# Kernel tuning notes

Hardware: AMD Instinct MI355X
Metric: run time of the kernel (lower is better)

The kernel has to match this reference:

```python
import jax, jax.numpy as jnp
import numpy as np

BS, HS, NH = 8, 3, 8          # block_size, halo_size, num_heads
WIN = BS + 2 * HS             # 14
DQK = 16                      # dim_head_qk = make_divisible(128*1.0)//8
DV = 16                       # dim_head_v = 128 // 8
SCALE = DQK ** -0.5


def _rel_pos_index():
    # Faithful numpy port of QueryFreePosEmbedRel._get_relative_position_index
    w = WIN
    coords = np.stack(np.meshgrid(np.arange(w), np.arange(w), indexing='ij'))  # (2,w,w)
    flat = coords.reshape(2, -1)                                               # (2, w*w)
    rel = flat[:, :, None] - flat[:, None, :]                                  # (2, ww, ww)
    rel = rel.transpose(1, 2, 0).astype(np.int64)
    rel[:, :, 0] += w - 1
    rel[:, :, 1] += w - 1
    rel[:, :, 0] *= 2 * w - 1
    rel = rel.sum(-1).reshape(w, w, w, w)
    sh = (w - BS) // 2  # == halo_size
    rel = rel[sh:sh + BS, sh:sh + BS, :, :].reshape(BS * BS, w * w)
    return rel

_REL_IDX = _rel_pos_index()


def setup_inputs() -> dict:
    key = jax.random.key(0)
    k1, k2, k3, k4, k5, k6 = jax.random.split(key, 6)
    C = 128
    dim_out_qk = NH * DQK   # 128
    dim_out_v = NH * DV     # 128
    x = jax.random.normal(k1, (4, 128, 128, C), dtype=jnp.float32)
    q_w = jax.random.normal(k2, (dim_out_qk, C), dtype=jnp.float32) * 0.05
    kv_w = jax.random.normal(k3, (dim_out_qk + dim_out_v, C), dtype=jnp.float32) * 0.05
    pos_table = jax.random.normal(k4, ((2 * WIN - 1) * (2 * WIN - 1), NH), dtype=jnp.float32) * 0.02
    proj_w = jax.random.normal(k5, (dim_out_v, dim_out_v), dtype=jnp.float32) * 0.05
    proj_b = jax.random.normal(k6, (dim_out_v,), dtype=jnp.float32) * 0.01
    return {"x": x, "q_w": q_w, "kv_w": kv_w, "pos_table": pos_table,
            "proj_w": proj_w, "proj_b": proj_b}


def reference(x, q_w, kv_w, pos_table, proj_w, proj_b):
    B, H, W, C = x.shape  # H,W divisible by BS -> no padding branch
    nhb, nwb = H // BS, W // BS
    nb = nhb * nwb

    # --- queries: (B,NH,nb,bs^2,DQK), block-partitioned ---
    q = x @ q_w.T
    q = q.reshape(B, nhb, BS, nwb, BS, NH, DQK).transpose(0, 5, 1, 3, 2, 4, 6)
    q = q.reshape(B, NH, nb, BS * BS, DQK)

    # --- kv 1x1 conv + halo padding + overlapping window extraction ---
    kv = x @ kv_w.T                                   # (B,H,W, NH*(DQK+DV))
    kv = jnp.pad(kv, ((0, 0), (HS, HS), (HS, HS), (0, 0)))
    ri = (np.arange(nhb) * BS)[:, None] + np.arange(WIN)[None, :]
    ci = (np.arange(nwb) * BS)[:, None] + np.arange(WIN)[None, :]
    kvw = kv[:, ri]
    kvw = kvw[:, :, :, ci]
    kvw = kvw.transpose(0, 1, 3, 2, 4, 5).reshape(B, nb, WIN * WIN, NH, DQK + DV)
    kvw = kvw.transpose(0, 3, 1, 2, 4)
    k = kvw[..., :DQK]
    v = kvw[..., DQK:]

    bias = pos_table[_REL_IDX.reshape(-1)].reshape(BS * BS, WIN * WIN, NH)
    bias = bias.transpose(2, 0, 1)[None, :, None]

    # --- scores + halo-boundary mask + softmax ---
    attn = jnp.einsum('bhnqd,bhnkd->bhnqk', q * SCALE, k) + bias
    ones = jnp.pad(jnp.ones((H, W), jnp.float32), ((HS, HS), (HS, HS)))
    mw = ones[ri][:, :, ci].transpose(0, 2, 1, 3).reshape(nb, WIN * WIN)
    valid = (mw > 0)[None, None, :, None, :]
    attn = jnp.where(valid, attn, -jnp.finfo(attn.dtype).max)
    attn = jax.nn.softmax(attn, axis=-1)

    # --- weighted sum over V, fold blocks back to (B,H,W,dim_out_v) ---
    out = jnp.einsum('bhnqk,bhnkd->bhnqd', attn, v)   # (B,NH,nb,bs^2,DV)
    out = out.reshape(B, NH, nhb, nwb, BS, BS, DV)
    out = out.transpose(0, 2, 4, 3, 5, 1, 6).reshape(B, H, W, NH * DV)
    return out @ proj_w.T + proj_b
```

## Files before the change

kernel.cpp:

```cpp
#include <hip/hip_runtime.h>
#include <float.h>


typedef float f32x4 __attribute__((ext_vector_type(4)));
typedef short s16x4 __attribute__((ext_vector_type(4)));
typedef short s16x8 __attribute__((ext_vector_type(8)));
typedef unsigned int u32x2 __attribute__((ext_vector_type(2)));
typedef unsigned int u32x4 __attribute__((ext_vector_type(4)));

__device__ inline ushort f2bf(float f) {
    unsigned u = __float_as_uint(f);
    return (ushort)((u + 0x7FFF + ((u >> 16) & 1)) >> 16);
}
__device__ inline float bf2f(ushort h) { return __uint_as_float((unsigned)h << 16); }
__device__ inline unsigned cvtpk(float a, float b) {
    unsigned r;
    asm("v_cvt_pk_bf16_f32 %0, %1, %2" : "=v"(r) : "v"(a), "v"(b));
    return r;
}
#if __has_builtin(__builtin_amdgcn_exp2f)
#define EXP2(x) __builtin_amdgcn_exp2f(x)
#else
#define EXP2(x) exp2f(x)
#endif

__global__ __launch_bounds__(256) void conv_w(
    const float* __restrict__ q_w, const float* __restrict__ kv_w,
    const float* __restrict__ proj_w, ushort* whi, ushort* wlo)
{
    const int g = blockIdx.x * 256 + threadIdx.x;
    const int row = g >> 7, col = g & 127;
    const float v = (row < 128) ? q_w[row * 128 + col]
                  : (row < 384) ? kv_w[(row - 128) * 128 + col]
                                : proj_w[(row - 384) * 128 + col];
    const ushort h = f2bf(v);
    whi[g] = h;
    wlo[g] = f2bf(v - bf2f(h));
}

__global__ __launch_bounds__(256) void gemm_split(
    const float* A,
    const ushort* __restrict__ Whi, const ushort* __restrict__ Wlo,
    int wbase, int ntc, int tok1,
    ushort* qb, ushort* kvb, float* outf, const float* __restrict__ bias)
{
    __shared__ ushort Ah[128 * 128];
    __shared__ ushort Al[128 * 128];

    const int t = threadIdx.x;
    const int row0 = blockIdx.x * 128;
    const int w = t >> 6, l = t & 63;
    const int wm = w >> 1, wn = w & 1;
    const int lr = l & 15, cA = l >> 4;

#pragma unroll
    for (int i = 0; i < 16; ++i) {
        const int idx = t + i * 256;
        const int p = idx >> 5, fc = idx & 31;
        const float4 v = *(const float4*)(A + (size_t)(row0 + p) * 128 + fc * 4);
        const int base = p * 128 + (((fc >> 1) ^ (p & 7)) << 3) + (fc & 1) * 4;
        const unsigned h01 = cvtpk(v.x, v.y), h23 = cvtpk(v.z, v.w);
        *(u32x2*)&Ah[base] = (u32x2){h01, h23};
        const float hx = __uint_as_float(h01 << 16);
        const float hy = __uint_as_float(h01 & 0xFFFF0000u);
        const float hz = __uint_as_float(h23 << 16);
        const float hw = __uint_as_float(h23 & 0xFFFF0000u);
        *(u32x2*)&Al[base] = (u32x2){ cvtpk(v.x - hx, v.y - hy),
                                      cvtpk(v.z - hz, v.w - hw) };
    }
    __syncthreads();

#pragma unroll 1
    for (int nt = 0; nt < ntc; ++nt) {
        f32x4 acc[4][4];
#pragma unroll
        for (int mf = 0; mf < 4; ++mf)
#pragma unroll
            for (int nf = 0; nf < 4; ++nf) acc[mf][nf] = (f32x4){0.f,0.f,0.f,0.f};

#pragma unroll 1
        for (int kk = 0; kk < 4; ++kk) {
            s16x8 wh[4], wl[4];
#pragma unroll
            for (int nf = 0; nf < 4; ++nf) {
                const size_t off = (size_t)(wbase + nt * 128 + wn * 64 + nf * 16 + lr) * 128
                                 + kk * 32 + cA * 8;
                wh[nf] = *(const s16x8*)&Whi[off];
                wl[nf] = *(const s16x8*)&Wlo[off];
            }
#pragma unroll
            for (int mf = 0; mf < 4; ++mf) {
                const int p = wm * 64 + mf * 16 + lr;
                const int off = p * 128 + ((((kk << 2) + cA) ^ (p & 7)) << 3);
                const s16x8 xh = *(const s16x8*)&Ah[off];
                const s16x8 xl = *(const s16x8*)&Al[off];
#pragma unroll
                for (int nf = 0; nf < 4; ++nf) {
                    acc[mf][nf] = __builtin_amdgcn_mfma_f32_16x16x32_bf16(
                                      wh[nf], xh, acc[mf][nf], 0, 0, 0);
                    acc[mf][nf] = __builtin_amdgcn_mfma_f32_16x16x32_bf16(
                                      wh[nf], xl, acc[mf][nf], 0, 0, 0);
                    acc[mf][nf] = __builtin_amdgcn_mfma_f32_16x16x32_bf16(
                                      wl[nf], xh, acc[mf][nf], 0, 0, 0);
                }
            }
        }

#pragma unroll
        for (int mf = 0; mf < 4; ++mf) {
            const size_t pix = row0 + wm * 64 + mf * 16 + lr;
#pragma unroll
            for (int nf = 0; nf < 4; ++nf) {
                const int chan = wn * 64 + nf * 16 + cA * 4;
                const f32x4 o = acc[mf][nf];
                if (tok1) {
                    const u32x2 pk = (u32x2){ cvtpk(o[0], o[1]), cvtpk(o[2], o[3]) };
                    if (nt == 0) {
                        const int head = wn * 4 + nf;
                        *(u32x2*)(qb + ((size_t)head << 20) + pix * 16 + (chan & 15)) = pk;
                    } else {
                        const int gchan = (nt - 1) * 128 + chan;
                        const int head = gchan >> 5;
                        *(u32x2*)(kvb + ((size_t)head << 21) + pix * 32 + (gchan & 31)) = pk;
                    }
                } else {
                    const float4 bv = *(const float4*)(bias + chan);
                    f32x4 r = o;
                    r[0] += bv.x; r[1] += bv.y; r[2] += bv.z; r[3] += bv.w;
                    *(f32x4*)(outf + pix * 128 + chan) = r;
                }
            }
        }
    }
}

__global__ __launch_bounds__(256) void halo_attn(
    float* out,
    const ushort* __restrict__ qg,
    const ushort* __restrict__ kvg,
    const float* __restrict__ pos_table)
{
    __shared__ ushort VT[4][16][232];
    __shared__ float  bias_l[648];
    __shared__ int    keyoff[256];
    __shared__ short  koff2[224];

    const int t  = threadIdx.x;
    const int bi = blockIdx.x, head = blockIdx.y;
    const int by = bi >> 4, bx = bi & 15;
    const int w  = t >> 6;
    const int l  = t & 63;
    const int lr = l & 15;
    const int cA = l >> 4;

    const char* kvh = (const char*)(kvg + ((size_t)head << 21) + ((size_t)w << 19));

    if (t < 224) {
        const int wy = t / 14, wx = t - (t / 14) * 14;
        const int py = by * 8 + wy - 3, px = bx * 8 + wx - 3;
        const bool valid = (t < 196) && ((unsigned)py < 128u) && ((unsigned)px < 128u);
        keyoff[t] = valid ? ((py * 128 + px) * 64) : 0;
        koff2[t]  = valid ? (short)(wy * 21 + wx) : (short)(-200);
    } else {
        keyoff[t] = 0;
    }
    for (int i = t; i < 648; i += 256) {
        if (i < 441) {
            const int ry = i / 21, rx = i - ry * 21;
            bias_l[i] = pos_table[((ry + 3) * 27 + rx + 3) * 8 + head] * 1.44269504f;
        } else {
            bias_l[i] = -30000.0f;
        }
    }
    __syncthreads();

    {
        const char* base = kvh + 32;
#pragma unroll 1
        for (int idx = l; idx < 112; idx += 64) {
            const char* s0 = base + keyoff[2 * idx];
            const char* s1 = base + keyoff[2 * idx + 1];
            const s16x8 a0 = *(const s16x8*)s0;
            const s16x8 a1 = *(const s16x8*)(s0 + 16);
            const s16x8 c0 = *(const s16x8*)s1;
            const s16x8 c1 = *(const s16x8*)(s1 + 16);
#pragma unroll
            for (int j = 0; j < 8; ++j) {
                *(unsigned*)&VT[w][j][2 * idx] =
                    ((unsigned)(ushort)c0[j] << 16) | (ushort)a0[j];
                *(unsigned*)&VT[w][j + 8][2 * idx] =
                    ((unsigned)(ushort)c1[j] << 16) | (ushort)a1[j];
            }
        }
    }
    __syncthreads();

    const int gbase = ((lr >> 2) << 3) + (lr & 3);
    const ushort* qh = qg + ((size_t)head << 20);
    s16x8 qf[4];
    float* optr[4];
    int qoff2[4];
#pragma unroll
    for (int qt = 0; qt < 4; ++qt) {
        const int q = qt * 16 + lr;
        const int qy = q >> 3, qx = q & 7;
        const size_t pix = ((size_t)(w * 128 + by * 8 + qy)) * 128 + bx * 8 + qx;
        optr[qt] = out + pix * 128 + head * 16 + cA * 4;
        qoff2[qt] = (qy + 13) * 21 + (qx + 13);
#pragma unroll
        for (int j = 0; j < 8; ++j) qf[qt][j] = 0;
        if (cA < 2)
            qf[qt] = *(const s16x8*)(qh + pix * 16 + cA * 8);
    }

    f32x4 accv[4];
    float sumf[4];
#pragma unroll
    for (int qt = 0; qt < 4; ++qt) {
        accv[qt] = (f32x4){0.f, 0.f, 0.f, 0.f};
        sumf[qt] = 0.f;
    }

    s16x8 ak0 = *(const s16x8*)(kvh + keyoff[gbase]     + cA * 16);
    s16x8 ak1 = *(const s16x8*)(kvh + keyoff[gbase + 4] + cA * 16);

#pragma unroll 1
    for (int m = 0; m < 7; ++m) {
        const int nx = 32 * (m + 1) + gbase;
        const s16x8 nk0 = *(const s16x8*)(kvh + keyoff[nx]     + cA * 16);
        const s16x8 nk1 = *(const s16x8*)(kvh + keyoff[nx + 4] + cA * 16);

        const int kb = 32 * m + cA * 8;
        const s16x8 kk = *(const s16x8*)&koff2[kb];
        const s16x8 vt = *(const s16x8*)&VT[w][lr][kb];

#pragma unroll
        for (int qt = 0; qt < 4; ++qt) {
            const f32x4 sf0 = __builtin_amdgcn_mfma_f32_16x16x32_bf16(
                                  ak0, qf[qt], (f32x4){0.f, 0.f, 0.f, 0.f}, 0, 0, 0);
            const f32x4 sf1 = __builtin_amdgcn_mfma_f32_16x16x32_bf16(
                                  ak1, qf[qt], (f32x4){0.f, 0.f, 0.f, 0.f}, 0, 0, 0);
            float pr0[4], pr1[4];
#pragma unroll
            for (int r = 0; r < 4; ++r)
                pr0[r] = EXP2(fmaf(sf0[r], 0.36067376f, bias_l[qoff2[qt] - (int)kk[r]]));
#pragma unroll
            for (int r = 0; r < 4; ++r)
                pr1[r] = EXP2(fmaf(sf1[r], 0.36067376f, bias_l[qoff2[qt] - (int)kk[4 + r]]));
            sumf[qt] += ((pr0[0] + pr0[1]) + (pr0[2] + pr0[3]))
                      + ((pr1[0] + pr1[1]) + (pr1[2] + pr1[3]));

            const u32x4 pk = (u32x4){ cvtpk(pr0[0], pr0[1]), cvtpk(pr0[2], pr0[3]),
                                      cvtpk(pr1[0], pr1[1]), cvtpk(pr1[2], pr1[3]) };
            const s16x8 pb = *(const s16x8*)&pk;
            accv[qt] = __builtin_amdgcn_mfma_f32_16x16x32_bf16(vt, pb, accv[qt], 0, 0, 0);
        }
        ak0 = nk0;
        ak1 = nk1;
    }

#pragma unroll
    for (int qt = 0; qt < 4; ++qt) {
        float s = sumf[qt];
        s += __shfl_xor(s, 16);
        s += __shfl_xor(s, 32);
        const float inv = 1.0f / s;
        *(f32x4*)optr[qt] = accv[qt] * inv;
    }
}

extern "C" void kernel_launch(void* const* d_in, const int* in_sizes, int n_in,
                              void* d_out, int out_size, void* d_ws, size_t ws_size,
                              hipStream_t stream) {
    const float* x      = (const float*)d_in[0];
    const float* q_w    = (const float*)d_in[1];
    const float* kv_w   = (const float*)d_in[2];
    const float* pt     = (const float*)d_in[3];
    const float* proj_w = (const float*)d_in[4];
    const float* proj_b = (const float*)d_in[5];
    float* out = (float*)d_out;

    ushort* ykvb = (ushort*)d_ws;
    ushort* qb   = (ushort*)((char*)d_ws + 33554432);
    ushort* whi  = (ushort*)((char*)d_ws + 33554432 + 16777216);
    ushort* wlo  = whi + 65536;

    const dim3 blk(256);
    conv_w<<<dim3(256), blk, 0, stream>>>(q_w, kv_w, proj_w, whi, wlo);
    gemm_split<<<dim3(512), blk, 0, stream>>>(x, whi, wlo, 0, 3, 1,
                                              qb, ykvb, nullptr, nullptr);
    halo_attn<<<dim3(256, 8), blk, 0, stream>>>(out, qb, ykvb, pt);
    gemm_split<<<dim3(512), blk, 0, stream>>>(out, whi, wlo, 384, 1, 0,
                                              nullptr, nullptr, out, proj_b);
}
```

Baseline: 105.8 us.

## Split halo attention across more blocks and tile weight layout for coalesced loads

The attention kernel launches twice as many blocks: each block now covers two batches, and each pair of waves splits the 64 queries of a window in half. Per-wave query tiles drop from four to two, raising parallelism and occupancy at the cost of recomputing the per-block bias and offset tables twice as often. Separately, the bf16 weight copies are written in a 16x8-tiled layout so each lane's 16-byte weight fetch in the GEMM lands contiguously per 16-row group, aiming to coalesce global weight loads.

Measured after the change: 94.13 us. 11.0% less time.

```diff
diff --git a/kernel.cpp b/kernel.cpp
--- a/kernel.cpp
+++ b/kernel.cpp
@@ -34,8 +34,9 @@
                   : (row < 384) ? kv_w[(row - 128) * 128 + col]
                                 : proj_w[(row - 384) * 128 + col];
     const ushort h = f2bf(v);
-    whi[g] = h;
-    wlo[g] = f2bf(v - bf2f(h));
+    const int off = ((row >> 4) * 2048) + ((col >> 3) * 128) + ((row & 15) * 8) + (col & 7);
+    whi[off] = h;
+    wlo[off] = f2bf(v - bf2f(h));
 }
 
 __global__ __launch_bounds__(256) void gemm_split(
@@ -83,8 +84,8 @@
             s16x8 wh[4], wl[4];
 #pragma unroll
             for (int nf = 0; nf < 4; ++nf) {
-                const size_t off = (size_t)(wbase + nt * 128 + wn * 64 + nf * 16 + lr) * 128
-                                 + kk * 32 + cA * 8;
+                const int rb = (wbase >> 4) + nt * 8 + wn * 4 + nf;
+                const size_t off = (size_t)rb * 2048 + (kk * 4 + cA) * 128 + lr * 8;
                 wh[nf] = *(const s16x8*)&Whi[off];
                 wl[nf] = *(const s16x8*)&Wlo[off];
             }
@@ -140,20 +141,23 @@
     const ushort* __restrict__ kvg,
     const float* __restrict__ pos_table)
 {
-    __shared__ ushort VT[4][16][232];
+    __shared__ ushort VT[2][16][232];
     __shared__ float  bias_l[648];
     __shared__ int    keyoff[256];
     __shared__ short  koff2[224];
 
     const int t  = threadIdx.x;
-    const int bi = blockIdx.x, head = blockIdx.y;
+    const int bi = blockIdx.x, head = blockIdx.y, bp = blockIdx.z;
     const int by = bi >> 4, bx = bi & 15;
     const int w  = t >> 6;
+    const int lb = w >> 1;
+    const int qh = w & 1;
+    const int batch = bp * 2 + lb;
     const int l  = t & 63;
     const int lr = l & 15;
     const int cA = l >> 4;
 
-    const char* kvh = (const char*)(kvg + ((size_t)head << 21) + ((size_t)w << 19));
+    const char* kvh = (const char*)(kvg + ((size_t)head << 21) + ((size_t)batch << 19));
 
     if (t < 224) {
         const int wy = t / 14, wx = t - (t / 14) * 14;
@@ -175,20 +179,20 @@
     __syncthreads();
 
     {
-        const char* base = kvh + 32;
-#pragma unroll 1
-        for (int idx = l; idx < 112; idx += 64) {
-            const char* s0 = base + keyoff[2 * idx];
-            const char* s1 = base + keyoff[2 * idx + 1];
+        const int l2 = qh * 64 + l;
+        if (l2 < 112) {
+            const char* base = kvh + 32;
+            const char* s0 = base + keyoff[2 * l2];
+            const char* s1 = base + keyoff[2 * l2 + 1];
             const s16x8 a0 = *(const s16x8*)s0;
             const s16x8 a1 = *(const s16x8*)(s0 + 16);
             const s16x8 c0 = *(const s16x8*)s1;
             const s16x8 c1 = *(const s16x8*)(s1 + 16);
 #pragma unroll
             for (int j = 0; j < 8; ++j) {
-                *(unsigned*)&VT[w][j][2 * idx] =
+                *(unsigned*)&VT[lb][j][2 * l2] =
                     ((unsigned)(ushort)c0[j] << 16) | (ushort)a0[j];
-                *(unsigned*)&VT[w][j + 8][2 * idx] =
+                *(unsigned*)&VT[lb][j + 8][2 * l2] =
                     ((unsigned)(ushort)c1[j] << 16) | (ushort)a1[j];
             }
         }
@@ -196,29 +200,29 @@
     __syncthreads();
 
     const int gbase = ((lr >> 2) << 3) + (lr & 3);
-    const ushort* qh = qg + ((size_t)head << 20);
-    s16x8 qf[4];
-    float* optr[4];
-    int qoff2[4];
-#pragma unroll
-    for (int qt = 0; qt < 4; ++qt) {
-        const int q = qt * 16 + lr;
+    const ushort* qhp = qg + ((size_t)head << 20);
+    s16x8 qf[2];
+    float* optr[2];
+    int qoff2[2];
+#pragma unroll
+    for (int j = 0; j < 2; ++j) {
+        const int q = (qh * 2 + j) * 16 + lr;
         const int qy = q >> 3, qx = q & 7;
-        const size_t pix = ((size_t)(w * 128 + by * 8 + qy)) * 128 + bx * 8 + qx;
-        optr[qt] = out + pix * 128 + head * 16 + cA * 4;
-        qoff2[qt] = (qy + 13) * 21 + (qx + 13);
-#pragma unroll
-        for (int j = 0; j < 8; ++j) qf[qt][j] = 0;
+        const size_t pix = ((size_t)(batch * 128 + by * 8 + qy)) * 128 + bx * 8 + qx;
+        optr[j] = out + pix * 128 + head * 16 + cA * 4;
+        qoff2[j] = (qy + 13) * 21 + (qx + 13);
+#pragma unroll
+        for (int k = 0; k < 8; ++k) qf[j][k] = 0;
         if (cA < 2)
-            qf[qt] = *(const s16x8*)(qh + pix * 16 + cA * 8);
-    }
-
-    f32x4 accv[4];
-    float sumf[4];
-#pragma unroll
-    for (int qt = 0; qt < 4; ++qt) {
-        accv[qt] = (f32x4){0.f, 0.f, 0.f, 0.f};
-        sumf[qt] = 0.f;
+            qf[j] = *(const s16x8*)(qhp + pix * 16 + cA * 8);
+    }
+
+    f32x4 accv[2];
+    float sumf[2];
+#pragma unroll
+    for (int j = 0; j < 2; ++j) {
+        accv[j] = (f32x4){0.f, 0.f, 0.f, 0.f};
+        sumf[j] = 0.f;
     }
 
     s16x8 ak0 = *(const s16x8*)(kvh + keyoff[gbase]     + cA * 16);
@@ -232,40 +236,40 @@
 
         const int kb = 32 * m + cA * 8;
         const s16x8 kk = *(const s16x8*)&koff2[kb];
-        const s16x8 vt = *(const s16x8*)&VT[w][lr][kb];
-
-#pragma unroll
-        for (int qt = 0; qt < 4; ++qt) {
+        const s16x8 vt = *(const s16x8*)&VT[lb][lr][kb];
+
+#pragma unroll
+        for (int j = 0; j < 2; ++j) {
             const f32x4 sf0 = __builtin_amdgcn_mfma_f32_16x16x32_bf16(
-                                  ak0, qf[qt], (f32x4){0.f, 0.f, 0.f, 0.f}, 0, 0, 0);
+                                  ak0, qf[j], (f32x4){0.f, 0.f, 0.f, 0.f}, 0, 0, 0);
             const f32x4 sf1 = __builtin_amdgcn_mfma_f32_16x16x32_bf16(
-                                  ak1, qf[qt], (f32x4){0.f, 0.f, 0.f, 0.f}, 0, 0, 0);
+                                  ak1, qf[j], (f32x4){0.f, 0.f, 0.f, 0.f}, 0, 0, 0);
             float pr0[4], pr1[4];
 #pragma unroll
             for (int r = 0; r < 4; ++r)
-                pr0[r] = EXP2(fmaf(sf0[r], 0.36067376f, bias_l[qoff2[qt] - (int)kk[r]]));
+                pr0[r] = EXP2(fmaf(sf0[r], 0.36067376f, bias_l[qoff2[j] - (int)kk[r]]));
 #pragma unroll
             for (int r = 0; r < 4; ++r)
-                pr1[r] = EXP2(fmaf(sf1[r], 0.36067376f, bias_l[qoff2[qt] - (int)kk[4 + r]]));
-            sumf[qt] += ((pr0[0] + pr0[1]) + (pr0[2] + pr0[3]))
-                      + ((pr1[0] + pr1[1]) + (pr1[2] + pr1[3]));
+                pr1[r] = EXP2(fmaf(sf1[r], 0.36067376f, bias_l[qoff2[j] - (int)kk[4 + r]]));
+            sumf[j] += ((pr0[0] + pr0[1]) + (pr0[2] + pr0[3]))
+                     + ((pr1[0] + pr1[1]) + (pr1[2] + pr1[3]));
 
             const u32x4 pk = (u32x4){ cvtpk(pr0[0], pr0[1]), cvtpk(pr0[2], pr0[3]),
                                       cvtpk(pr1[0], pr1[1]), cvtpk(pr1[2], pr1[3]) };
             const s16x8 pb = *(const s16x8*)&pk;
-            accv[qt] = __builtin_amdgcn_mfma_f32_16x16x32_bf16(vt, pb, accv[qt], 0, 0, 0);
+            accv[j] = __builtin_amdgcn_mfma_f32_16x16x32_bf16(vt, pb, accv[j], 0, 0, 0);
         }
         ak0 = nk0;
         ak1 = nk1;
     }
 
 #pragma unroll
-    for (int qt = 0; qt < 4; ++qt) {
-        float s = sumf[qt];
+    for (int j = 0; j < 2; ++j) {
+        float s = sumf[j];
         s += __shfl_xor(s, 16);
         s += __shfl_xor(s, 32);
         const float inv = 1.0f / s;
-        *(f32x4*)optr[qt] = accv[qt] * inv;
+        *(f32x4*)optr[j] = accv[j] * inv;
     }
 }
 
@@ -289,7 +293,7 @@
     conv_w<<<dim3(256), blk, 0, stream>>>(q_w, kv_w, proj_w, whi, wlo);
     gemm_split<<<dim3(512), blk, 0, stream>>>(x, whi, wlo, 0, 3, 1,
                                               qb, ykvb, nullptr, nullptr);
-    halo_attn<<<dim3(256, 8), blk, 0, stream>>>(out, qb, ykvb, pt);
+    halo_attn<<<dim3(256, 8, 2), blk, 0, stream>>>(out, qb, ykvb, pt);
     gemm_split<<<dim3(512), blk, 0, stream>>>(out, whi, wlo, 384, 1, 0,
                                               nullptr, nullptr, out, proj_b);
 }
```
